# Kernel tuning notes

Measured on AMD Instinct MI355X. Metric: run time of the kernel, lower is better.

Reference implementation:

```python
import jax, jax.numpy as jnp
import numpy as np

BN = 100000
E = 1600000
C1 = 64
C2 = 64


def setup_inputs() -> dict:
    key = jax.random.key(0)
    k1, k2, k3, k4 = jax.random.split(key, 4)
    x = jax.random.normal(k1, (BN, C1), dtype=jnp.float32)
    e_ = jax.random.randint(k2, (2, E), 0, BN, dtype=jnp.int64)
    # nn.Linear(C1, C2): y = x @ W^T + b; store W pre-transposed as (C1, C2)
    W = jax.random.normal(k3, (C1, C2), dtype=jnp.float32) * (1.0 / np.sqrt(C1))
    b = jax.random.normal(k4, (C2,), dtype=jnp.float32) * 0.01
    return {"x": x, "e_": e_, "W": W, "b": b}


def reference(x, e_, W, b):
    bn = x.shape[0]
    row, col = e_[0], e_[1]
    # deg = bincount(row); deg^{-1/2} with inf -> 0
    deg = jax.ops.segment_sum(jnp.ones(row.shape, dtype=x.dtype), row, num_segments=bn)
    deg_inv_sqrt = jnp.where(deg > 0, jnp.power(jnp.maximum(deg, 1.0), -0.5), 0.0)
    norm = deg_inv_sqrt[row] * deg_inv_sqrt[col]          # (E,)
    h = x @ W + b                                         # (BN, C2)
    messages = norm[:, None] * h[row]                     # (E, C2) gather + scale
    y = jax.ops.segment_sum(messages, col, num_segments=bn)  # scatter-add over dst
    return y
```

## Files before the change

kernel.cpp:

```cpp
#include <hip/hip_runtime.h>
#include <hip/hip_bf16.h>

#define C 64
#define CPB 256
#define NBUCKC 391
#define CAPC 5120
#define RPB 1024
#define NBUCKR 98
#define CAPR 20480
#define EPB 4096
#define PAD 16

typedef __attribute__((ext_vector_type(8))) short bf16x8;
typedef __attribute__((ext_vector_type(4))) float f32x4;

__device__ __forceinline__ unsigned short f2bf(float f) {
    __hip_bfloat16 h = __float2bfloat16(f);
    return *(unsigned short*)&h;
}

__device__ __forceinline__ int seg_find(const int* seg, int n, int i) {
    int lo = 0, hi = n;
    while (hi - lo > 1) {
        int mid = (lo + hi) >> 1;
        if (seg[mid] <= i) lo = mid; else hi = mid;
    }
    return lo;
}

__global__ __launch_bounds__(512) void partA_kernel(const int* __restrict__ row,
                                                    const int* __restrict__ col,
                                                    int* __restrict__ bcurC,
                                                    int* __restrict__ bcurR,
                                                    int* __restrict__ stageC,
                                                    unsigned short* __restrict__ stageR,
                                                    int ne) {
    __shared__ int buf[EPB];
    __shared__ int cC[NBUCKC], segC[NBUCKC + 1], dC[NBUCKC];
    __shared__ int cR[NBUCKR], segR[NBUCKR + 1], dR[NBUCKR];
    const int tid = threadIdx.x;
    const int lane = tid & 63, wid = tid >> 6;

    for (int i = tid; i < NBUCKC; i += 512) cC[i] = 0;
    if (tid < NBUCKR) cR[tid] = 0;
    __syncthreads();

    const int s = blockIdx.x * EPB, e = min(s + EPB, ne);
    const int nloc = e - s;
    int rr[8], cc[8];
#pragma unroll
    for (int u = 0; u < 8; ++u) {
        int i = s + tid + u * 512;
        if (i < e) { rr[u] = row[i]; cc[u] = col[i]; }
        else { rr[u] = -1; cc[u] = -1; }
    }
#pragma unroll
    for (int u = 0; u < 8; ++u) {
        if (cc[u] >= 0) {
            atomicAdd(&cC[cc[u] >> 8], 1);
            atomicAdd(&cR[rr[u] >> 10], 1);
        }
    }
    __syncthreads();
    if (wid == 0) {
        int carry = 0;
        for (int base = 0; base < NBUCKC; base += 64) {
            int idx = base + lane;
            int v = (idx < NBUCKC) ? cC[idx] : 0;
            int x = v;
#pragma unroll
            for (int off = 1; off < 64; off <<= 1) {
                int t = __shfl_up(x, off, 64);
                if (lane >= off) x += t;
            }
            if (idx < NBUCKC) segC[idx] = carry + x - v;
            carry += __shfl(x, 63, 64);
        }
        if (lane == 0) segC[NBUCKC] = carry;
    } else if (wid == 1) {
        int carry = 0;
        for (int base = 0; base < NBUCKR; base += 64) {
            int idx = base + lane;
            int v = (idx < NBUCKR) ? cR[idx] : 0;
            int x = v;
#pragma unroll
            for (int off = 1; off < 64; off <<= 1) {
                int t = __shfl_up(x, off, 64);
                if (lane >= off) x += t;
            }
            if (idx < NBUCKR) segR[idx] = carry + x - v;
            carry += __shfl(x, 63, 64);
        }
        if (lane == 0) segR[NBUCKR] = carry;
    }
    __syncthreads();
    for (int t = tid; t < NBUCKC; t += 512) {
        int cnt = cC[t];
        dC[t] = t * CAPC + atomicAdd(&bcurC[t * PAD], cnt) - segC[t];
        cC[t] = segC[t];
    }
    if (tid < NBUCKR) {
        int cnt = cR[tid];
        dR[tid] = tid * CAPR + atomicAdd(&bcurR[tid * PAD], cnt) - segR[tid];
        cR[tid] = segR[tid];
    }
    __syncthreads();
#pragma unroll
    for (int u = 0; u < 8; ++u) {
        if (cc[u] >= 0) {
            int bk = cc[u] >> 8;
            int lpos = atomicAdd(&cC[bk], 1);
            buf[lpos] = ((cc[u] & 255) << 17) | rr[u];
        }
    }
    __syncthreads();
    for (int i = tid; i < nloc; i += 512) {
        int b = seg_find(segC, NBUCKC, i);
        int dst = dC[b] + i;
        if (dst < (b + 1) * CAPC) stageC[dst] = buf[i];
    }
    __syncthreads();
#pragma unroll
    for (int u = 0; u < 8; ++u) {
        if (rr[u] >= 0) {
            int rb = rr[u] >> 10;
            int lpos = atomicAdd(&cR[rb], 1);
            buf[lpos] = rr[u];
        }
    }
    __syncthreads();
    for (int i = tid; i < nloc; i += 512) {
        int b = seg_find(segR, NBUCKR, i);
        int dst = dR[b] + i;
        if (dst < (b + 1) * CAPR) stageR[dst] = (unsigned short)(buf[i] & (RPB - 1));
    }
}

__global__ __launch_bounds__(512) void fusedB_kernel(const int* __restrict__ bcC,
                                                     const int* __restrict__ bcR,
                                                     const int* __restrict__ stageC,
                                                     const unsigned short* __restrict__ stageR,
                                                     float* __restrict__ dis,
                                                     int* __restrict__ offs,
                                                     int* __restrict__ srcs,
                                                     int bn, int ne) {
    __shared__ int hist[CPB];
    __shared__ int dhist[RPB];
    __shared__ int wv8[8];
    __shared__ int wsum[4];
    __shared__ int sbase_s;
    const int b = blockIdx.x, tid = threadIdx.x;
    const int lane = tid & 63, wid = tid >> 6;

    if (b < NBUCKR) {
        for (int i = tid; i < RPB; i += 512) dhist[i] = 0;
        __syncthreads();
        const int sbR = b * CAPR;
        const int cntR = min(bcR[b * PAD], CAPR);
        for (int j = tid; j < cntR; j += 512) atomicAdd(&dhist[stageR[sbR + j]], 1);
        __syncthreads();
        for (int i = tid; i < RPB; i += 512) {
            int r = b * RPB + i;
            if (r < bn) {
                int d = dhist[i];
                dis[r] = d > 0 ? rsqrtf((float)d) : 0.0f;
            }
        }
    }
    int part = 0;
    for (int t = tid; t < b; t += 512) part += min(bcC[t * PAD], CAPC);
#pragma unroll
    for (int off = 32; off >= 1; off >>= 1) part += __shfl_xor(part, off, 64);
    if (lane == 0) wv8[wid] = part;
    __syncthreads();
    if (tid == 0) {
        int s = 0;
#pragma unroll
        for (int k = 0; k < 8; ++k) s += wv8[k];
        sbase_s = s;
    }
    if (tid < CPB) hist[tid] = 0;
    __syncthreads();
    const int sbase = sbase_s;
    const int sbC = b * CAPC;
    const int cntC = min(bcC[b * PAD], CAPC);
    for (int j = tid; j < cntC; j += 512) atomicAdd(&hist[stageC[sbC + j] >> 17], 1);
    __syncthreads();
    int v = 0, x = 0;
    if (tid < CPB) {
        v = hist[tid];
        x = v;
#pragma unroll
        for (int off = 1; off < 64; off <<= 1) {
            int t = __shfl_up(x, off, 64);
            if (lane >= off) x += t;
        }
        if (lane == 63) wsum[wid] = x;
    }
    __syncthreads();
    if (tid == 0) {
        int a = 0;
#pragma unroll
        for (int k = 0; k < 4; ++k) { int t = wsum[k]; wsum[k] = a; a += t; }
    }
    __syncthreads();
    if (tid < CPB) {
        int excl = (x - v) + wsum[wid];
        int c = b * CPB + tid;
        if (c < bn) offs[c] = sbase + excl;
        hist[tid] = sbase + excl;
    }
    __syncthreads();
    for (int j = tid; j < cntC; j += 512) {
        int val = stageC[sbC + j];
        int pos = atomicAdd(&hist[val >> 17], 1);
        srcs[pos] = val & 0x1FFFF;
    }
    if (b == NBUCKC - 1 && tid == 0) offs[bn] = sbase + cntC;
}

__global__ __launch_bounds__(256) void linear_mfma_kernel(const float* __restrict__ x,
                                                          const float* __restrict__ W,
                                                          const float* __restrict__ b,
                                                          const float* __restrict__ dis,
                                                          __hip_bfloat16* __restrict__ hb,
                                                          int bn) {
    __shared__ unsigned short xb[64][72];
    __shared__ unsigned short Wt[64][72];
    __shared__ float bs[64];
    __shared__ float dss[64];
    const int t = threadIdx.x;
    const int R0 = blockIdx.x * 64;

    {
        int row = t >> 2, q = t & 3;
        int grow = R0 + row;
        float4 vv[4];
        if (grow < bn) {
            const float4* xp = (const float4*)(x + (size_t)grow * C + q * 16);
#pragma unroll
            for (int i = 0; i < 4; ++i) vv[i] = xp[i];
        } else {
#pragma unroll
            for (int i = 0; i < 4; ++i) vv[i] = make_float4(0.f, 0.f, 0.f, 0.f);
        }
#pragma unroll
        for (int i = 0; i < 4; ++i) {
            unsigned short* d = &xb[row][q * 16 + i * 4];
            d[0] = f2bf(vv[i].x); d[1] = f2bf(vv[i].y);
            d[2] = f2bf(vv[i].z); d[3] = f2bf(vv[i].w);
        }
    }
    {
        int k = t >> 2, q = t & 3;
        const float* wp = W + (size_t)k * C + q * 16;
#pragma unroll
        for (int j = 0; j < 16; ++j) Wt[q * 16 + j][k] = f2bf(wp[j]);
    }
    if (t < 64) bs[t] = b[t];
    else if (t < 128) { int i = t - 64; int g = R0 + i; dss[i] = (g < bn) ? dis[g] : 0.f; }
    __syncthreads();

    const int wv = t >> 6;
    const int l = t & 63;
    const int lm = l & 15;
    const int g = l >> 4;

    const bf16x8 a0 = *(const bf16x8*)&xb[wv * 16 + lm][g * 8];
    const bf16x8 a1 = *(const bf16x8*)&xb[wv * 16 + lm][32 + g * 8];

#pragma unroll
    for (int n = 0; n < 4; ++n) {
        const bf16x8 b0 = *(const bf16x8*)&Wt[n * 16 + lm][g * 8];
        const bf16x8 b1 = *(const bf16x8*)&Wt[n * 16 + lm][32 + g * 8];
        float bias = bs[n * 16 + lm];
        f32x4 acc = {bias, bias, bias, bias};
        acc = __builtin_amdgcn_mfma_f32_16x16x32_bf16(a0, b0, acc, 0, 0, 0);
        acc = __builtin_amdgcn_mfma_f32_16x16x32_bf16(a1, b1, acc, 0, 0, 0);
#pragma unroll
        for (int reg = 0; reg < 4; ++reg) {
            int lrow = wv * 16 + g * 4 + reg;
            int grow = R0 + lrow;
            if (grow < bn)
                hb[(size_t)grow * C + n * 16 + lm] = __float2bfloat16(dss[lrow] * acc[reg]);
        }
    }
}

__device__ __forceinline__ float bf_lo(unsigned int p) { return __uint_as_float(p << 16); }
__device__ __forceinline__ float bf_hi(unsigned int p) { return __uint_as_float(p & 0xFFFF0000u); }

__global__ void gather_kernel(const int* __restrict__ offs, const int* __restrict__ srcs,
                              const uint2* __restrict__ hb64,
                              const float* __restrict__ dis,
                              float* __restrict__ y, int bn) {
    int r = blockIdx.x * (blockDim.x >> 6) + (threadIdx.x >> 6);
    if (r >= bn) return;
    const int lane = threadIdx.x & 63;
    const int q = lane >> 4;
    const int cq = lane & 15;
    const int s0 = offs[r], e0 = offs[r + 1];
    float4 acc = {0.f, 0.f, 0.f, 0.f};
    for (int base = s0; base < e0; base += 64) {
        int j = base + lane;
        int srcv = (j < e0) ? srcs[j] : 0;
        int cnt = min(64, e0 - base);
        int t = 0;
        for (; t + 16 <= cnt; t += 16) {
            int a0 = __shfl(srcv, t + q, 64);
            int a1 = __shfl(srcv, t + 4 + q, 64);
            int a2 = __shfl(srcv, t + 8 + q, 64);
            int a3 = __shfl(srcv, t + 12 + q, 64);
            uint2 p0 = hb64[(size_t)a0 * 16 + cq];
            uint2 p1 = hb64[(size_t)a1 * 16 + cq];
            uint2 p2 = hb64[(size_t)a2 * 16 + cq];
            uint2 p3 = hb64[(size_t)a3 * 16 + cq];
            acc.x += bf_lo(p0.x); acc.y += bf_hi(p0.x); acc.z += bf_lo(p0.y); acc.w += bf_hi(p0.y);
            acc.x += bf_lo(p1.x); acc.y += bf_hi(p1.x); acc.z += bf_lo(p1.y); acc.w += bf_hi(p1.y);
            acc.x += bf_lo(p2.x); acc.y += bf_hi(p2.x); acc.z += bf_lo(p2.y); acc.w += bf_hi(p2.y);
            acc.x += bf_lo(p3.x); acc.y += bf_hi(p3.x); acc.z += bf_lo(p3.y); acc.w += bf_hi(p3.y);
        }
        for (; t + 4 <= cnt; t += 4) {
            int a = __shfl(srcv, t + q, 64);
            uint2 p = hb64[(size_t)a * 16 + cq];
            acc.x += bf_lo(p.x); acc.y += bf_hi(p.x); acc.z += bf_lo(p.y); acc.w += bf_hi(p.y);
        }
        if (t < cnt) {
            int idx = t + q;
            int a = __shfl(srcv, idx & 63, 64);
            if (idx < cnt) {
                uint2 p = hb64[(size_t)a * 16 + cq];
                acc.x += bf_lo(p.x); acc.y += bf_hi(p.x); acc.z += bf_lo(p.y); acc.w += bf_hi(p.y);
            }
        }
    }
    acc.x += __shfl_xor(acc.x, 16, 64); acc.y += __shfl_xor(acc.y, 16, 64);
    acc.z += __shfl_xor(acc.z, 16, 64); acc.w += __shfl_xor(acc.w, 16, 64);
    acc.x += __shfl_xor(acc.x, 32, 64); acc.y += __shfl_xor(acc.y, 32, 64);
    acc.z += __shfl_xor(acc.z, 32, 64); acc.w += __shfl_xor(acc.w, 32, 64);
    if (q == 0) {
        float d = dis[r];
        float4 out = {acc.x * d, acc.y * d, acc.z * d, acc.w * d};
        *reinterpret_cast<float4*>(y + (size_t)r * C + 4 * cq) = out;
    }
}

extern "C" void kernel_launch(void* const* d_in, const int* in_sizes, int n_in,
                              void* d_out, int out_size, void* d_ws, size_t ws_size,
                              hipStream_t stream) {
    const float* x = (const float*)d_in[0];
    const int*   e = (const int*)d_in[1];
    const float* W = (const float*)d_in[2];
    const float* b = (const float*)d_in[3];
    float* y = (float*)d_out;

    const int bn = in_sizes[0] / C;
    const int ne = in_sizes[1] / 2;

    const int* rowi = e;
    const int* coli = e + ne;

    char* ws = (char*)d_ws;
    float* dis   = (float*)ws;  ws += (size_t)bn * 4;
    int*   offs  = (int*)ws;    ws += ((size_t)bn + 4) * 4;
    int*   bcC   = (int*)ws;    ws += (size_t)NBUCKC * PAD * 4;
    int*   bcR   = (int*)ws;    ws += (size_t)NBUCKR * PAD * 4;
    int*   srcs  = (int*)ws;    ws += (size_t)ne * 4;
    int*            stageC = (int*)ws;            ws += (size_t)NBUCKC * CAPC * 4;
    unsigned short* stageR = (unsigned short*)ws; ws += (size_t)NBUCKR * CAPR * 2;
    __hip_bfloat16* hb = (__hip_bfloat16*)ws;

    hipMemsetAsync(bcC, 0, (size_t)(NBUCKC + NBUCKR) * PAD * 4, stream);

    const int nchunks = (ne + EPB - 1) / EPB;
    partA_kernel<<<nchunks, 512, 0, stream>>>(rowi, coli, bcC, bcR, stageC, stageR, ne);
    fusedB_kernel<<<NBUCKC, 512, 0, stream>>>(bcC, bcR, stageC, stageR, dis, offs, srcs, bn, ne);
    linear_mfma_kernel<<<(bn + 63) / 64, 256, 0, stream>>>(x, W, b, dis, hb, bn);
    gather_kernel<<<(bn + 3) / 4, 256, 0, stream>>>(offs, srcs, (const uint2*)hb, dis, y, bn);
}
```

Baseline: 119.0 us.

## Fuse per-bucket CSR build into gather kernel using shared-memory sorted sources

Splits the old fused bucket kernel into a degree-only kernel over row buckets, and moves the per-column-bucket counting sort into the gather kernel. The sort now writes source indices into shared memory instead of global srcs/offs, removing a global round trip and the prefix-sum across buckets. The cost is a grid of only 391 blocks of 512 threads each doing gathers for 256 destination rows, with large shared usage (~22KB), which reduces parallelism and may leave many CUs idle or load-imbalanced.

```diff
diff --git a/kernel.cpp b/kernel.cpp
--- a/kernel.cpp
+++ b/kernel.cpp
@@ -136,87 +136,24 @@
     }
 }
 
-__global__ __launch_bounds__(512) void fusedB_kernel(const int* __restrict__ bcC,
-                                                     const int* __restrict__ bcR,
-                                                     const int* __restrict__ stageC,
-                                                     const unsigned short* __restrict__ stageR,
-                                                     float* __restrict__ dis,
-                                                     int* __restrict__ offs,
-                                                     int* __restrict__ srcs,
-                                                     int bn, int ne) {
-    __shared__ int hist[CPB];
-    __shared__ int dhist[RPB];
-    __shared__ int wv8[8];
-    __shared__ int wsum[4];
-    __shared__ int sbase_s;
+__global__ __launch_bounds__(512) void degK_kernel(const int* __restrict__ bcR,
+                                                   const unsigned short* __restrict__ stageR,
+                                                   float* __restrict__ dis, int bn) {
+    __shared__ int dh[RPB];
     const int b = blockIdx.x, tid = threadIdx.x;
-    const int lane = tid & 63, wid = tid >> 6;
-
-    if (b < NBUCKR) {
-        for (int i = tid; i < RPB; i += 512) dhist[i] = 0;
-        __syncthreads();
-        const int sbR = b * CAPR;
-        const int cntR = min(bcR[b * PAD], CAPR);
-        for (int j = tid; j < cntR; j += 512) atomicAdd(&dhist[stageR[sbR + j]], 1);
-        __syncthreads();
-        for (int i = tid; i < RPB; i += 512) {
-            int r = b * RPB + i;
-            if (r < bn) {
-                int d = dhist[i];
-                dis[r] = d > 0 ? rsqrtf((float)d) : 0.0f;
-            }
-        }
-    }
-    int part = 0;
-    for (int t = tid; t < b; t += 512) part += min(bcC[t * PAD], CAPC);
-#pragma unroll
-    for (int off = 32; off >= 1; off >>= 1) part += __shfl_xor(part, off, 64);
-    if (lane == 0) wv8[wid] = part;
-    __syncthreads();
-    if (tid == 0) {
-        int s = 0;
-#pragma unroll
-        for (int k = 0; k < 8; ++k) s += wv8[k];
-        sbase_s = s;
-    }
-    if (tid < CPB) hist[tid] = 0;
-    __syncthreads();
-    const int sbase = sbase_s;
-    const int sbC = b * CAPC;
-    const int cntC = min(bcC[b * PAD], CAPC);
-    for (int j = tid; j < cntC; j += 512) atomicAdd(&hist[stageC[sbC + j] >> 17], 1);
-    __syncthreads();
-    int v = 0, x = 0;
-    if (tid < CPB) {
-        v = hist[tid];
-        x = v;
-#pragma unroll
-        for (int off = 1; off < 64; off <<= 1) {
-            int t = __shfl_up(x, off, 64);
-            if (lane >= off) x += t;
-        }
-        if (lane == 63) wsum[wid] = x;
-    }
-    __syncthreads();
-    if (tid == 0) {
-        int a = 0;
-#pragma unroll
-        for (int k = 0; k < 4; ++k) { int t = wsum[k]; wsum[k] = a; a += t; }
-    }
-    __syncthreads();
-    if (tid < CPB) {
-        int excl = (x - v) + wsum[wid];
-        int c = b * CPB + tid;
-        if (c < bn) offs[c] = sbase + excl;
-        hist[tid] = sbase + excl;
-    }
-    __syncthreads();
-    for (int j = tid; j < cntC; j += 512) {
-        int val = stageC[sbC + j];
-        int pos = atomicAdd(&hist[val >> 17], 1);
-        srcs[pos] = val & 0x1FFFF;
-    }
-    if (b == NBUCKC - 1 && tid == 0) offs[bn] = sbase + cntC;
+    for (int i = tid; i < RPB; i += 512) dh[i] = 0;
+    __syncthreads();
+    const int sb = b * CAPR;
+    const int cnt = min(bcR[b * PAD], CAPR);
+    for (int j = tid; j < cnt; j += 512) atomicAdd(&dh[stageR[sb + j]], 1);
+    __syncthreads();
+    for (int i = tid; i < RPB; i += 512) {
+        int r = b * RPB + i;
+        if (r < bn) {
+            int d = dh[i];
+            dis[r] = d > 0 ? rsqrtf((float)d) : 0.0f;
+        }
+    }
 }
 
 __global__ __launch_bounds__(256) void linear_mfma_kernel(const float* __restrict__ x,
@@ -290,58 +227,104 @@
 __device__ __forceinline__ float bf_lo(unsigned int p) { return __uint_as_float(p << 16); }
 __device__ __forceinline__ float bf_hi(unsigned int p) { return __uint_as_float(p & 0xFFFF0000u); }
 
-__global__ void gather_kernel(const int* __restrict__ offs, const int* __restrict__ srcs,
-                              const uint2* __restrict__ hb64,
-                              const float* __restrict__ dis,
-                              float* __restrict__ y, int bn) {
-    int r = blockIdx.x * (blockDim.x >> 6) + (threadIdx.x >> 6);
-    if (r >= bn) return;
-    const int lane = threadIdx.x & 63;
-    const int q = lane >> 4;
-    const int cq = lane & 15;
-    const int s0 = offs[r], e0 = offs[r + 1];
-    float4 acc = {0.f, 0.f, 0.f, 0.f};
-    for (int base = s0; base < e0; base += 64) {
-        int j = base + lane;
-        int srcv = (j < e0) ? srcs[j] : 0;
-        int cnt = min(64, e0 - base);
-        int t = 0;
-        for (; t + 16 <= cnt; t += 16) {
-            int a0 = __shfl(srcv, t + q, 64);
-            int a1 = __shfl(srcv, t + 4 + q, 64);
-            int a2 = __shfl(srcv, t + 8 + q, 64);
-            int a3 = __shfl(srcv, t + 12 + q, 64);
-            uint2 p0 = hb64[(size_t)a0 * 16 + cq];
-            uint2 p1 = hb64[(size_t)a1 * 16 + cq];
-            uint2 p2 = hb64[(size_t)a2 * 16 + cq];
-            uint2 p3 = hb64[(size_t)a3 * 16 + cq];
-            acc.x += bf_lo(p0.x); acc.y += bf_hi(p0.x); acc.z += bf_lo(p0.y); acc.w += bf_hi(p0.y);
-            acc.x += bf_lo(p1.x); acc.y += bf_hi(p1.x); acc.z += bf_lo(p1.y); acc.w += bf_hi(p1.y);
-            acc.x += bf_lo(p2.x); acc.y += bf_hi(p2.x); acc.z += bf_lo(p2.y); acc.w += bf_hi(p2.y);
-            acc.x += bf_lo(p3.x); acc.y += bf_hi(p3.x); acc.z += bf_lo(p3.y); acc.w += bf_hi(p3.y);
-        }
-        for (; t + 4 <= cnt; t += 4) {
-            int a = __shfl(srcv, t + q, 64);
-            uint2 p = hb64[(size_t)a * 16 + cq];
-            acc.x += bf_lo(p.x); acc.y += bf_hi(p.x); acc.z += bf_lo(p.y); acc.w += bf_hi(p.y);
-        }
-        if (t < cnt) {
-            int idx = t + q;
-            int a = __shfl(srcv, idx & 63, 64);
-            if (idx < cnt) {
+__global__ __launch_bounds__(512) void gatherB_kernel(const int* __restrict__ bcC,
+                                                      const int* __restrict__ stageC,
+                                                      const uint2* __restrict__ hb64,
+                                                      const float* __restrict__ dis,
+                                                      float* __restrict__ y, int bn) {
+    __shared__ int buf[CAPC];
+    __shared__ int seg[CPB + 1];
+    __shared__ int cur[CPB];
+    __shared__ int wsum[4];
+    const int b = blockIdx.x, tid = threadIdx.x;
+    const int lane = tid & 63, wid = tid >> 6;
+
+    if (tid < CPB) cur[tid] = 0;
+    __syncthreads();
+    const int sb = b * CAPC;
+    const int cnt = min(bcC[b * PAD], CAPC);
+    for (int j = tid; j < cnt; j += 512) atomicAdd(&cur[stageC[sb + j] >> 17], 1);
+    __syncthreads();
+    int v = 0, x = 0;
+    if (tid < CPB) {
+        v = cur[tid];
+        x = v;
+#pragma unroll
+        for (int off = 1; off < 64; off <<= 1) {
+            int t = __shfl_up(x, off, 64);
+            if (lane >= off) x += t;
+        }
+        if (lane == 63) wsum[wid] = x;
+    }
+    __syncthreads();
+    if (tid == 0) {
+        int a = 0;
+#pragma unroll
+        for (int k = 0; k < 4; ++k) { int t = wsum[k]; wsum[k] = a; a += t; }
+    }
+    __syncthreads();
+    if (tid < CPB) {
+        int excl = (x - v) + wsum[wid];
+        seg[tid] = excl;
+        cur[tid] = excl;
+    }
+    if (tid == 0) seg[CPB] = cnt;
+    __syncthreads();
+    for (int j = tid; j < cnt; j += 512) {
+        int val = stageC[sb + j];
+        int p = atomicAdd(&cur[val >> 17], 1);
+        buf[p] = val & 0x1FFFF;
+    }
+    __syncthreads();
+
+    const int q = lane >> 4, cq = lane & 15;
+    for (int dl = wid * 32; dl < wid * 32 + 32; ++dl) {
+        int grow = b * CPB + dl;
+        if (grow >= bn) break;
+        const int s0 = seg[dl], e0 = seg[dl + 1];
+        float4 acc = {0.f, 0.f, 0.f, 0.f};
+        for (int base = s0; base < e0; base += 64) {
+            int j = base + lane;
+            int srcv = (j < e0) ? buf[j] : 0;
+            int m = min(64, e0 - base);
+            int t = 0;
+            for (; t + 16 <= m; t += 16) {
+                int a0 = __shfl(srcv, t + q, 64);
+                int a1 = __shfl(srcv, t + 4 + q, 64);
+                int a2 = __shfl(srcv, t + 8 + q, 64);
+                int a3 = __shfl(srcv, t + 12 + q, 64);
+                uint2 p0 = hb64[(size_t)a0 * 16 + cq];
+                uint2 p1 = hb64[(size_t)a1 * 16 + cq];
+                uint2 p2 = hb64[(size_t)a2 * 16 + cq];
+                uint2 p3 = hb64[(size_t)a3 * 16 + cq];
+                acc.x += bf_lo(p0.x); acc.y += bf_hi(p0.x); acc.z += bf_lo(p0.y); acc.w += bf_hi(p0.y);
+                acc.x += bf_lo(p1.x); acc.y += bf_hi(p1.x); acc.z += bf_lo(p1.y); acc.w += bf_hi(p1.y);
+                acc.x += bf_lo(p2.x); acc.y += bf_hi(p2.x); acc.z += bf_lo(p2.y); acc.w += bf_hi(p2.y);
+                acc.x += bf_lo(p3.x); acc.y += bf_hi(p3.x); acc.z += bf_lo(p3.y); acc.w += bf_hi(p3.y);
+            }
+            for (; t + 4 <= m; t += 4) {
+                int a = __shfl(srcv, t + q, 64);
                 uint2 p = hb64[(size_t)a * 16 + cq];
                 acc.x += bf_lo(p.x); acc.y += bf_hi(p.x); acc.z += bf_lo(p.y); acc.w += bf_hi(p.y);
             }
-        }
-    }
-    acc.x += __shfl_xor(acc.x, 16, 64); acc.y += __shfl_xor(acc.y, 16, 64);
-    acc.z += __shfl_xor(acc.z, 16, 64); acc.w += __shfl_xor(acc.w, 16, 64);
-    acc.x += __shfl_xor(acc.x, 32, 64); acc.y += __shfl_xor(acc.y, 32, 64);
-    acc.z += __shfl_xor(acc.z, 32, 64); acc.w += __shfl_xor(acc.w, 32, 64);
-    if (q == 0) {
-        float d = dis[r];
-        float4 out = {acc.x * d, acc.y * d, acc.z * d, acc.w * d};
-        *reinterpret_cast<float4*>(y + (size_t)r * C + 4 * cq) = out;
+            if (t < m) {
+                int idx = t + q;
+                int a = __shfl(srcv, idx & 63, 64);
+                if (idx < m) {
+                    uint2 p = hb64[(size_t)a * 16 + cq];
+                    acc.x += bf_lo(p.x); acc.y += bf_hi(p.x); acc.z += bf_lo(p.y); acc.w += bf_hi(p.y);
+                }
+            }
+        }
+        acc.x += __shfl_xor(acc.x, 16, 64); acc.y += __shfl_xor(acc.y, 16, 64);
+        acc.z += __shfl_xor(acc.z, 16, 64); acc.w += __shfl_xor(acc.w, 16, 64);
+        acc.x += __shfl_xor(acc.x, 32, 64); acc.y += __shfl_xor(acc.y, 32, 64);
+        acc.z += __shfl_xor(acc.z, 32, 64); acc.w += __shfl_xor(acc.w, 32, 64);
+        if (q == 0) {
+            float d = dis[grow];
+            float4 out = {acc.x * d, acc.y * d, acc.z * d, acc.w * d};
+            *reinterpret_cast<float4*>(y + (size_t)grow * C + 4 * cq) = out;
+        }
     }
 }
 
@@ -362,10 +345,8 @@
 
     char* ws = (char*)d_ws;
     float* dis   = (float*)ws;  ws += (size_t)bn * 4;
-    int*   offs  = (int*)ws;    ws += ((size_t)bn + 4) * 4;
     int*   bcC   = (int*)ws;    ws += (size_t)NBUCKC * PAD * 4;
     int*   bcR   = (int*)ws;    ws += (size_t)NBUCKR * PAD * 4;
-    int*   srcs  = (int*)ws;    ws += (size_t)ne * 4;
     int*            stageC = (int*)ws;            ws += (size_t)NBUCKC * CAPC * 4;
     unsigned short* stageR = (unsigned short*)ws; ws += (size_t)NBUCKR * CAPR * 2;
     __hip_bfloat16* hb = (__hip_bfloat16*)ws;
@@ -374,7 +355,7 @@
 
     const int nchunks = (ne + EPB - 1) / EPB;
     partA_kernel<<<nchunks, 512, 0, stream>>>(rowi, coli, bcC, bcR, stageC, stageR, ne);
-    fusedB_kernel<<<NBUCKC, 512, 0, stream>>>(bcC, bcR, stageC, stageR, dis, offs, srcs, bn, ne);
+    degK_kernel<<<NBUCKR, 512, 0, stream>>>(bcR, stageR, dis, bn);
     linear_mfma_kernel<<<(bn + 63) / 64, 256, 0, stream>>>(x, W, b, dis, hb, bn);
-    gather_kernel<<<(bn + 3) / 4, 256, 0, stream>>>(offs, srcs, (const uint2*)hb, dis, y, bn);
-}
+    gatherB_kernel<<<NBUCKC, 512, 0, stream>>>(bcC, stageC, (const uint2*)hb, dis, y, bn);
+}
```

Result: slower. 128.5 us (+8.0%).
